# Performance work log

Hardware: AMD Instinct MI355X
Metric: run time of the kernel (lower is better)

## Reference

```python
import jax, jax.numpy as jnp
import numpy as np

B, L, HID, H, D = 1, 2048, 3072, 24, 128
MLP = 4 * HID
LH, LW = 32, 56      # latent mask grid -> LH*LW image tokens at the END of the sequence
LIP = 16             # IP-adapter image tokens
IP_SCALE = 0.6


def setup_inputs() -> dict:
    key = jax.random.key(0)
    k = jax.random.split(key, 10)
    # Flux rotary pe layout [1,1,L,D//2,2,2]: pe[...,0]=[cos,-sin], pe[...,1]=[sin,cos]
    pos = jnp.arange(L, dtype=jnp.float32)
    freqs = 1.0 / (10000.0 ** (jnp.arange(0, D, 2, dtype=jnp.float32) / D))
    ang = pos[:, None] * freqs[None, :]            # [L, D//2]
    cos, sin = jnp.cos(ang), jnp.sin(ang)
    pe = jnp.stack([jnp.stack([cos, -sin], -1), jnp.stack([sin, cos], -1)], -2)[None, None]
    return {
        "x": jax.random.normal(k[0], (B, L, HID), jnp.float32),
        "vec": jax.random.normal(k[1], (B, HID), jnp.float32),
        "pe": pe,
        "img_mask": jax.random.uniform(k[2], (B, LH, LW), jnp.float32),
        "image_emb": jax.random.normal(k[3], (B, LIP, HID), jnp.float32),
        "mod_w": jax.random.normal(k[4], (3 * HID, HID), jnp.float32) * 0.02,
        "mod_b": jnp.zeros((3 * HID,), jnp.float32),
        "lin1_w": jax.random.normal(k[5], (3 * HID + MLP, HID), jnp.float32) * 0.02,
        "lin1_b": jnp.zeros((3 * HID + MLP,), jnp.float32),
        "q_scale": jnp.ones((D,), jnp.float32),
        "k_scale": jnp.ones((D,), jnp.float32),
        "lin2_w": jax.random.normal(k[6], (HID, HID + MLP), jnp.float32) * 0.02,
        "lin2_b": jnp.zeros((HID,), jnp.float32),
        "ipk_w": jax.random.normal(k[7], (HID, HID), jnp.float32) * 0.02,
        "ipv_w": jax.random.normal(k[8], (HID, HID), jnp.float32) * 0.02,
    }


def _rms(x, scale, eps):
    # RMSNorm over last dim (QKNorm / norm_added_k)
    return x * jax.lax.rsqrt(jnp.mean(x * x, -1, keepdims=True) + eps) * scale


def _apply_rope(x, pe):
    # x: [B,H,L,D]; pe: [1,1,L,D//2,2,2]
    xr = x.reshape(x.shape[:-1] + (D // 2, 1, 2))
    out = pe[..., 0] * xr[..., 0] + pe[..., 1] * xr[..., 1]  # [B,H,L,D//2,2]
    return out.reshape(x.shape)


def _sdpa(q, k, v):
    # q:[B,H,Lq,D] k,v:[B,H,Lk,D] -> [B,Lq,H*D]
    s = jnp.einsum('bhqd,bhkd->bhqk', q, k) / jnp.sqrt(jnp.float32(D))
    o = jnp.einsum('bhqk,bhkd->bhqd', jax.nn.softmax(s, -1), v)
    return o.transpose(0, 2, 1, 3).reshape(q.shape[0], q.shape[2], H * D)


def reference(x, vec, pe, img_mask, image_emb, mod_w, mod_b, lin1_w, lin1_b,
              q_scale, k_scale, lin2_w, lin2_b, ipk_w, ipv_w):
    # modulation: SiLU(vec) -> Linear -> (shift, scale, gate), each [B,1,HID]
    mod = jax.nn.silu(vec) @ mod_w.T + mod_b
    shift, scale, gate = [m[:, None, :] for m in jnp.split(mod, 3, -1)]
    # pre_norm: LayerNorm, no affine, eps 1e-6 (biased variance, matches torch)
    ln = (x - jnp.mean(x, -1, keepdims=True)) * jax.lax.rsqrt(jnp.var(x, -1, keepdims=True) + 1e-6)
    x_mod = (1.0 + scale) * ln + shift
    # fused qkv + mlp projection
    h = x_mod @ lin1_w.T + lin1_b
    qkv, mlp = h[..., :3 * HID], h[..., 3 * HID:]
    q, k, v = qkv.reshape(B, L, 3, H, D).transpose(2, 0, 3, 1, 4)  # each [B,H,L,D]
    q = _rms(q, q_scale, 1e-6)
    k = _rms(k, k_scale, 1e-6)
    # rp_attention: RoPE then SDPA
    attn = _sdpa(_apply_rope(q, pe), _apply_rope(k, pe), v)       # [B,L,HID]
    # IP-adapter cross-attention: pre-rope q attends to projected image_emb
    ip_k = _rms((image_emb @ ipk_w.T).reshape(B, LIP, H, D).transpose(0, 2, 1, 3), 1.0, 1e-5)
    ip_v = (image_emb @ ipv_w.T).reshape(B, LIP, H, D).transpose(0, 2, 1, 3)
    ip_h = IP_SCALE * _sdpa(q, ip_k, ip_v)                        # [B,L,HID]
    # spatial mask applied to last LH*LW tokens, zeros elsewhere
    full_mask = jnp.concatenate(
        [jnp.zeros((B, L - LH * LW), ip_h.dtype), img_mask.reshape(B, LH * LW)], 1)
    attn = attn + ip_h * full_mask[..., None]
    out = jnp.concatenate([attn, jax.nn.gelu(mlp, approximate=True)], -1) @ lin2_w.T + lin2_b
    return x + gate * out
```

## Files before the change

### kernel.cpp

```cpp
#include <hip/hip_runtime.h>

#define HID 3072
#define LSEQ 2048
#define NH 24
#define HD 128
#define N1 21504
#define K2 15360

typedef unsigned short ushort_t;
typedef __attribute__((ext_vector_type(8))) short bf16x8;
typedef __attribute__((ext_vector_type(4))) float f32x4;

__device__ __forceinline__ unsigned short f2bf(float f) {
    union { float f; unsigned int u; } v; v.f = f;
    unsigned int u = v.u;
    u += 0x7fffu + ((u >> 16) & 1u);
    return (unsigned short)(u >> 16);
}
__device__ __forceinline__ float bf2f(unsigned short s) {
    union { unsigned int u; float f; } v; v.u = ((unsigned int)s) << 16;
    return v.f;
}
__device__ __forceinline__ float gelu_tanh(float x) {
    float u = 0.7978845608028654f * (x + 0.044715f * x * x * x);
    float t = 2.0f / (1.0f + __expf(-2.0f * u)) - 1.0f;
    return 0.5f * x * (1.0f + t);
}
__device__ __forceinline__ void gload_lds16(const ushort_t* g, ushort_t* l) {
    __builtin_amdgcn_global_load_lds((const __attribute__((address_space(1))) void*)g,
                                     (__attribute__((address_space(3))) void*)l, 16, 0, 0);
}

__global__ __launch_bounds__(256) void k_cvt(const float* __restrict__ src,
    ushort_t* __restrict__ dst, int n)
{
    int stride = gridDim.x * 256 * 8;
    for (int i = (blockIdx.x * 256 + threadIdx.x) * 8; i < n; i += stride) {
        float4 a = *reinterpret_cast<const float4*>(src + i);
        float4 b = *reinterpret_cast<const float4*>(src + i + 4);
        uint4 pk;
        pk.x = (unsigned)f2bf(a.x) | ((unsigned)f2bf(a.y) << 16);
        pk.y = (unsigned)f2bf(a.z) | ((unsigned)f2bf(a.w) << 16);
        pk.z = (unsigned)f2bf(b.x) | ((unsigned)f2bf(b.y) << 16);
        pk.w = (unsigned)f2bf(b.z) | ((unsigned)f2bf(b.w) << 16);
        *reinterpret_cast<uint4*>(dst + i) = pk;
    }
}

__global__ __launch_bounds__(256) void k_mod(const float* __restrict__ vec,
    const float* __restrict__ mw, const float* __restrict__ mb, float* __restrict__ mod) {
    __shared__ __align__(16) float sv[HID];
    int tid = threadIdx.x;
    for (int i = tid; i < HID; i += 256) {
        float v = vec[i];
        sv[i] = v / (1.0f + __expf(-v));
    }
    __syncthreads();
    int wave = tid >> 6, lane = tid & 63;
    int n = blockIdx.x * 4 + wave;
    const float* w = mw + (size_t)n * HID;
    float acc = 0.0f;
    for (int k = lane * 4; k < HID; k += 256) {
        float4 wv = *reinterpret_cast<const float4*>(w + k);
        float4 s  = *reinterpret_cast<const float4*>(sv + k);
        acc += wv.x * s.x + wv.y * s.y + wv.z * s.z + wv.w * s.w;
    }
    #pragma unroll
    for (int off = 1; off < 64; off <<= 1) acc += __shfl_xor(acc, off);
    if (lane == 0) mod[n] = acc + mb[n];
}

__global__ __launch_bounds__(256) void k_lnmod(const float* __restrict__ x,
    const float* __restrict__ mod, ushort_t* __restrict__ xmod) {
    int row = blockIdx.x, tid = threadIdx.x;
    const float4* xr = reinterpret_cast<const float4*>(x + (size_t)row * HID);
    float4 v[3];
    float s = 0.f, sq = 0.f;
    #pragma unroll
    for (int i = 0; i < 3; ++i) {
        v[i] = xr[tid + i * 256];
        s  += v[i].x + v[i].y + v[i].z + v[i].w;
        sq += v[i].x * v[i].x + v[i].y * v[i].y + v[i].z * v[i].z + v[i].w * v[i].w;
    }
    #pragma unroll
    for (int off = 1; off < 64; off <<= 1) { s += __shfl_xor(s, off); sq += __shfl_xor(sq, off); }
    __shared__ float rs[4], rq[4];
    int wave = tid >> 6, lane = tid & 63;
    if (lane == 0) { rs[wave] = s; rq[wave] = sq; }
    __syncthreads();
    s  = rs[0] + rs[1] + rs[2] + rs[3];
    sq = rq[0] + rq[1] + rq[2] + rq[3];
    float mean = s * (1.0f / HID);
    float var = sq * (1.0f / HID) - mean * mean;
    float rstd = rsqrtf(var + 1e-6f);
    ushort_t* orow = xmod + (size_t)row * HID;
    #pragma unroll
    for (int i = 0; i < 3; ++i) {
        int c = (tid + i * 256) * 4;
        float4 sc = *reinterpret_cast<const float4*>(mod + HID + c);
        float4 sh = *reinterpret_cast<const float4*>(mod + c);
        float o0 = (1.f + sc.x) * ((v[i].x - mean) * rstd) + sh.x;
        float o1 = (1.f + sc.y) * ((v[i].y - mean) * rstd) + sh.y;
        float o2 = (1.f + sc.z) * ((v[i].z - mean) * rstd) + sh.z;
        float o3 = (1.f + sc.w) * ((v[i].w - mean) * rstd) + sh.w;
        *reinterpret_cast<ushort4*>(orow + c) = make_ushort4(f2bf(o0), f2bf(o1), f2bf(o2), f2bf(o3));
    }
}

template<int EPI>
__global__ __launch_bounds__(512) void k_gemm8(
    const ushort_t* __restrict__ A, const ushort_t* __restrict__ W,
    const float* __restrict__ bias, int Ks, int klen,
    ushort_t* __restrict__ out_qkv, ushort_t* __restrict__ out_concat,
    float* __restrict__ part)
{
    extern __shared__ __align__(16) char smem_raw[];
    ushort_t* smem = (ushort_t*)smem_raw;
    int tid = threadIdx.x;
    int wid = tid >> 6, l = tid & 63;
    int wm = wid >> 2, wn = wid & 3;
    int lr = l & 15, lg = l >> 4;

    int NTILE = (EPI == 1) ? 84 : 12;
    int flat = blockIdx.y * NTILE + blockIdx.x;
    int nf = (flat & 7) * NTILE + (flat >> 3);
    int mt = nf & 7, nt = nf >> 3;
    int m0 = mt * 256, n0 = nt * 256;
    int koff = blockIdx.z * klen;
    int NT = klen >> 6;

    int lrow = l >> 3;
    int lc   = (l & 7) ^ lrow;
    int arow_st = wm * 128 + wn * 32 + lrow;
    int bhalf = wn >> 1, ridx = wm * 2 + (wn & 1);
    int brow_st = bhalf * 128 + ridx * 32 + lrow;
    const ushort_t* aSrc = A + (size_t)(m0 + arow_st) * Ks + koff + lc * 8;
    const ushort_t* bSrc = W + (size_t)(n0 + brow_st) * Ks + koff + lc * 8;
    int aDst = (wm * 128 + wn * 32) * 64;
    int bDst = (bhalf * 128 + ridx * 32) * 64;

    auto stageA = [&](int t, int buf, int c) {
        gload_lds16(aSrc + (size_t)c * 8 * Ks + (size_t)t * 64,
                    smem + buf * 16384 + aDst + c * 512);
    };
    auto stageB = [&](int t, int c) {
        gload_lds16(bSrc + (size_t)c * 8 * Ks + (size_t)t * 64,
                    smem + 49152 + (t & 1) * 16384 + bDst + c * 512);
    };
    auto readA = [&](int buf, int row, int ccc) {
        return *reinterpret_cast<const bf16x8*>(smem + buf * 16384 + row * 64 + ((ccc ^ (row & 7)) << 3));
    };
    auto readB = [&](int p, int row, int ccc) {
        return *reinterpret_cast<const bf16x8*>(smem + 49152 + p * 16384 + row * 64 + ((ccc ^ (row & 7)) << 3));
    };

    f32x4 acc[8][4] = {};
    bf16x8 bfrag[4][2];

    #pragma unroll
    for (int c = 0; c < 4; ++c) stageA(0, 0, c);
    #pragma unroll
    for (int c = 0; c < 4; ++c) stageB(0, c);
    #pragma unroll
    for (int c = 0; c < 4; ++c) stageA(1, 1, c);
    #pragma unroll
    for (int c = 0; c < 4; ++c) stageB(1, c);
    asm volatile("s_waitcnt vmcnt(8)" ::: "memory");
    __builtin_amdgcn_s_barrier();

    int pA = 0;
    int pA2 = 2;
    for (int t = 0; t < NT; ++t) {
        int pB = t & 1;
        #pragma unroll
        for (int ph = 0; ph < 4; ++ph) {
            bf16x8 af[2][2];
            if (ph == 0) {
                #pragma unroll
                for (int nj = 0; nj < 4; ++nj)
                    #pragma unroll
                    for (int kh = 0; kh < 2; ++kh)
                        bfrag[nj][kh] = readB(pB, wn * 64 + nj * 16 + lr, kh * 4 + lg);
            }
            #pragma unroll
            for (int i = 0; i < 2; ++i)
                #pragma unroll
                for (int kh = 0; kh < 2; ++kh)
                    af[i][kh] = readA(pA, wm * 128 + (2 * ph + i) * 16 + lr, kh * 4 + lg);
            if (ph < 2) {
                if (t + 2 < NT) { stageA(t + 2, pA2, ph * 2); stageA(t + 2, pA2, ph * 2 + 1); }
            } else {
                if (t + 2 < NT) { stageB(t + 2, (ph - 2) * 2); stageB(t + 2, (ph - 2) * 2 + 1); }
            }
            __builtin_amdgcn_s_barrier();
            __builtin_amdgcn_s_setprio(1);
            #pragma unroll
            for (int i = 0; i < 2; ++i)
                #pragma unroll
                for (int nj = 0; nj < 4; ++nj)
                    #pragma unroll
                    for (int kh = 0; kh < 2; ++kh)
                        acc[2 * ph + i][nj] = __builtin_amdgcn_mfma_f32_16x16x32_bf16(
                            af[i][kh], bfrag[nj][kh], acc[2 * ph + i][nj], 0, 0, 0);
            __builtin_amdgcn_s_setprio(0);
            if (ph == 3 && t + 1 < NT) {
                if (t + 2 < NT) asm volatile("s_waitcnt vmcnt(8)" ::: "memory");
                else            asm volatile("s_waitcnt vmcnt(0)" ::: "memory");
            }
            __builtin_amdgcn_s_barrier();
        }
        pA  = (pA  + 1 == 3) ? 0 : pA  + 1;
        pA2 = (pA2 + 1 == 3) ? 0 : pA2 + 1;
    }

    #pragma unroll
    for (int nj = 0; nj < 4; ++nj) {
        int col = n0 + wn * 64 + nj * 16 + lr;
        float b = (EPI == 1) ? bias[col] : 0.f;
        #pragma unroll
        for (int mi = 0; mi < 8; ++mi) {
            int rbase = m0 + wm * 128 + mi * 16 + lg * 4;
            #pragma unroll
            for (int r = 0; r < 4; ++r) {
                int mrow = rbase + r;
                float val = acc[mi][nj][r] + b;
                if (EPI == 1) {
                    if (col < 3 * HID) {
                        out_qkv[(size_t)mrow * (3 * HID) + col] = f2bf(val);
                    } else {
                        out_concat[(size_t)mrow * K2 + HID + (col - 3 * HID)] = f2bf(gelu_tanh(val));
                    }
                } else {
                    part[(size_t)blockIdx.z * LSEQ * HID + (size_t)mrow * HID + col] = val;
                }
            }
        }
    }
}

__global__ __launch_bounds__(256) void k_red(const float* __restrict__ part,
    const float* __restrict__ bias, const float* __restrict__ xres,
    const float* __restrict__ mod, float* __restrict__ dout)
{
    size_t base = ((size_t)blockIdx.x * 256 + threadIdx.x) * 4;
    int col = (int)(base % HID);
    float4 p0 = *reinterpret_cast<const float4*>(part + base);
    float4 p1 = *reinterpret_cast<const float4*>(part + (size_t)LSEQ * HID + base);
    float4 bb = *reinterpret_cast<const float4*>(bias + col);
    float4 gg = *reinterpret_cast<const float4*>(mod + 2 * HID + col);
    float4 xx = *reinterpret_cast<const float4*>(xres + base);
    float4 o;
    o.x = xx.x + gg.x * (p0.x + p1.x + bb.x);
    o.y = xx.y + gg.y * (p0.y + p1.y + bb.y);
    o.z = xx.z + gg.z * (p0.z + p1.z + bb.z);
    o.w = xx.w + gg.w * (p0.w + p1.w + bb.w);
    *reinterpret_cast<float4*>(dout + base) = o;
}

__global__ __launch_bounds__(256) void k_qkv(const ushort_t* __restrict__ qkv,
    const float* __restrict__ pe, const float* __restrict__ q_scale, const float* __restrict__ k_scale,
    ushort_t* __restrict__ q_rope, ushort_t* __restrict__ k_rope,
    ushort_t* __restrict__ q_rms, ushort_t* __restrict__ v_t)
{
    __shared__ ushort_t vtile[64][132];
    int h = blockIdx.y, l0 = blockIdx.x * 64;
    int wave = threadIdx.x >> 6, lane = threadIdx.x & 63;
    int d0 = lane * 2;
    float qs0 = q_scale[d0], qs1 = q_scale[d0 + 1];
    float ks0 = k_scale[d0], ks1 = k_scale[d0 + 1];
    for (int it = 0; it < 16; ++it) {
        int ll = it * 4 + wave;
        int l = l0 + ll;
        const ushort_t* base = qkv + (size_t)l * (3 * HID) + h * HD + d0;
        unsigned qw = *reinterpret_cast<const unsigned*>(base);
        unsigned kw = *reinterpret_cast<const unsigned*>(base + HID);
        unsigned vw = *reinterpret_cast<const unsigned*>(base + 2 * HID);
        float qx = bf2f((ushort_t)(qw & 0xffffu)), qy = bf2f((ushort_t)(qw >> 16));
        float kx = bf2f((ushort_t)(kw & 0xffffu)), ky = bf2f((ushort_t)(kw >> 16));
        float sq = qx * qx + qy * qy;
        float sk = kx * kx + ky * ky;
        #pragma unroll
        for (int off = 1; off < 64; off <<= 1) { sq += __shfl_xor(sq, off); sk += __shfl_xor(sk, off); }
        float rqv = rsqrtf(sq * (1.0f / HD) + 1e-6f);
        float rkv = rsqrtf(sk * (1.0f / HD) + 1e-6f);
        float qnx = qx * rqv * qs0, qny = qy * rqv * qs1;
        float knx = kx * rkv * ks0, kny = ky * rkv * ks1;
        float4 p = *reinterpret_cast<const float4*>(pe + ((size_t)l * 64 + lane) * 4);
        size_t off_hl = ((size_t)h * LSEQ + l) * HD + d0;
        *reinterpret_cast<unsigned*>(q_rms + off_hl) = (unsigned)f2bf(qnx) | ((unsigned)f2bf(qny) << 16);
        float qrx = p.x * qnx + p.y * qny, qry = p.z * qnx + p.w * qny;
        float krx = p.x * knx + p.y * kny, kry = p.z * knx + p.w * kny;
        *reinterpret_cast<unsigned*>(q_rope + off_hl) = (unsigned)f2bf(qrx) | ((unsigned)f2bf(qry) << 16);
        *reinterpret_cast<unsigned*>(k_rope + off_hl) = (unsigned)f2bf(krx) | ((unsigned)f2bf(kry) << 16);
        vtile[ll][d0] = (ushort_t)(vw & 0xffffu);
        vtile[ll][d0 + 1] = (ushort_t)(vw >> 16);
    }
    __syncthreads();
    int d = threadIdx.x >> 1, half = threadIdx.x & 1;
    ushort_t* dst = v_t + ((size_t)h * HD + d) * LSEQ + l0 + half * 32;
    #pragma unroll
    for (int g = 0; g < 4; ++g) {
        unsigned w0, w1, w2, w3;
        int lb = half * 32 + g * 8;
        w0 = (unsigned)vtile[lb + 0][d] | ((unsigned)vtile[lb + 1][d] << 16);
        w1 = (unsigned)vtile[lb + 2][d] | ((unsigned)vtile[lb + 3][d] << 16);
        w2 = (unsigned)vtile[lb + 4][d] | ((unsigned)vtile[lb + 5][d] << 16);
        w3 = (unsigned)vtile[lb + 6][d] | ((unsigned)vtile[lb + 7][d] << 16);
        reinterpret_cast<uint4*>(dst)[g] = make_uint4(w0, w1, w2, w3);
    }
}

__global__ __launch_bounds__(256) void k_ipgemv(const float* __restrict__ emb,
    const float* __restrict__ wk, const float* __restrict__ wv,
    float* __restrict__ ipk, float* __restrict__ ipv)
{
    int task = blockIdx.x * 4 + (threadIdx.x >> 6);
    int lane = threadIdx.x & 63;
    int which = task / HID;
    int n = task % HID;
    const float* w = (which ? wv : wk) + (size_t)n * HID;
    float acc[16];
    #pragma unroll
    for (int t = 0; t < 16; ++t) acc[t] = 0.f;
    for (int k = lane; k < HID; k += 64) {
        float wval = w[k];
        #pragma unroll
        for (int t = 0; t < 16; ++t) acc[t] += emb[t * HID + k] * wval;
    }
    #pragma unroll
    for (int off = 1; off < 64; off <<= 1) {
        #pragma unroll
        for (int t = 0; t < 16; ++t) acc[t] += __shfl_xor(acc[t], off);
    }
    if (lane == 0) {
        int hh = n >> 7, d = n & 127;
        float* dstp = which ? ipv : ipk;
        #pragma unroll
        for (int t = 0; t < 16; ++t) dstp[((size_t)hh * 16 + t) * HD + d] = acc[t];
    }
}

__global__ __launch_bounds__(256) void k_ipkrms(float* __restrict__ ipk) {
    int row = blockIdx.x * 4 + (threadIdx.x >> 6);
    int lane = threadIdx.x & 63;
    float2 v = *reinterpret_cast<const float2*>(ipk + (size_t)row * HD + lane * 2);
    float sq = v.x * v.x + v.y * v.y;
    #pragma unroll
    for (int off = 1; off < 64; off <<= 1) sq += __shfl_xor(sq, off);
    float r = rsqrtf(sq * (1.0f / HD) + 1e-5f);
    float2 o; o.x = v.x * r; o.y = v.y * r;
    *reinterpret_cast<float2*>(ipk + (size_t)row * HD + lane * 2) = o;
}

__global__ __launch_bounds__(256) void k_attn(const ushort_t* __restrict__ q_rope,
    const ushort_t* __restrict__ k_rope, const ushort_t* __restrict__ v_t,
    float* __restrict__ attnbuf)
{
    __shared__ __align__(16) ushort_t Ks[32 * 128];
    __shared__ __align__(16) ushort_t Vs[128 * 32];
    __shared__ __align__(16) ushort_t Ps[4 * 32 * 40];
    const float SC = 0.08838834764831845f;
    int h = blockIdx.y, q0 = blockIdx.x * 128;
    int tid = threadIdx.x, wave = tid >> 6, lane = tid & 63;
    int lr = lane & 15, lg = lane >> 4;
    const ushort_t* Kb = k_rope + (size_t)h * LSEQ * HD;
    const ushort_t* Vb = v_t + (size_t)h * HD * LSEQ;
    bf16x8 qf[2][4];
    #pragma unroll
    for (int i = 0; i < 2; ++i) {
        #pragma unroll
        for (int ks = 0; ks < 4; ++ks) {
            int row = q0 + wave * 32 + i * 16 + lr;
            int d = ks * 32 + lg * 8;
            qf[i][ks] = *reinterpret_cast<const bf16x8*>(q_rope + ((size_t)h * LSEQ + row) * HD + d);
        }
    }
    f32x4 o[2][8] = {};
    float mrun[2][4], lrun[2][4];
    #pragma unroll
    for (int i = 0; i < 2; ++i)
        #pragma unroll
        for (int r = 0; r < 4; ++r) { mrun[i][r] = -1e30f; lrun[i][r] = 0.f; }

    for (int kt = 0; kt < LSEQ; kt += 32) {
        #pragma unroll
        for (int ii = 0; ii < 2; ++ii) {
            int c = tid + ii * 256;
            int krow = c >> 4, kc = c & 15;
            uint4 va = *reinterpret_cast<const uint4*>(Kb + (size_t)(kt + krow) * HD + kc * 8);
            *reinterpret_cast<uint4*>(reinterpret_cast<char*>(Ks) + krow * 256 + ((kc ^ (krow & 15)) << 4)) = va;
            int dr = c >> 2, vc = c & 3;
            uint4 vb = *reinterpret_cast<const uint4*>(Vb + (size_t)dr * LSEQ + kt + vc * 8);
            *reinterpret_cast<uint4*>(reinterpret_cast<char*>(Vs) + dr * 64 + ((vc ^ ((dr >> 1) & 3)) << 4)) = vb;
        }
        __syncthreads();
        f32x4 s[2][2] = {};
        #pragma unroll
        for (int ks = 0; ks < 4; ++ks) {
            bf16x8 kf[2];
            #pragma unroll
            for (int j = 0; j < 2; ++j) {
                int krow = j * 16 + lr;
                int cc = ks * 4 + lg;
                kf[j] = *reinterpret_cast<const bf16x8*>(reinterpret_cast<char*>(Ks) + krow * 256 + ((cc ^ (krow & 15)) << 4));
            }
            #pragma unroll
            for (int i = 0; i < 2; ++i)
                #pragma unroll
                for (int j = 0; j < 2; ++j)
                    s[i][j] = __builtin_amdgcn_mfma_f32_16x16x32_bf16(qf[i][ks], kf[j], s[i][j], 0, 0, 0);
        }
        float alpha[2][4];
        #pragma unroll
        for (int i = 0; i < 2; ++i) {
            #pragma unroll
            for (int r = 0; r < 4; ++r) {
                float v0 = s[i][0][r] * SC, v1 = s[i][1][r] * SC;
                float mx = fmaxf(v0, v1);
                #pragma unroll
                for (int off = 1; off < 16; off <<= 1) mx = fmaxf(mx, __shfl_xor(mx, off));
                float mnew = fmaxf(mrun[i][r], mx);
                float al = __expf(mrun[i][r] - mnew);
                float p0 = __expf(v0 - mnew), p1 = __expf(v1 - mnew);
                float rs2 = p0 + p1;
                #pragma unroll
                for (int off = 1; off < 16; off <<= 1) rs2 += __shfl_xor(rs2, off);
                lrun[i][r] = lrun[i][r] * al + rs2;
                mrun[i][r] = mnew;
                alpha[i][r] = al;
                s[i][0][r] = p0; s[i][1][r] = p1;
            }
        }
        #pragma unroll
        for (int i = 0; i < 2; ++i)
            #pragma unroll
            for (int j8 = 0; j8 < 8; ++j8)
                #pragma unroll
                for (int r = 0; r < 4; ++r) o[i][j8][r] *= alpha[i][r];
        #pragma unroll
        for (int i = 0; i < 2; ++i)
            #pragma unroll
            for (int j = 0; j < 2; ++j)
                #pragma unroll
                for (int r = 0; r < 4; ++r) {
                    int ql = i * 16 + lg * 4 + r;
                    int kp = j * 16 + lr;
                    Ps[wave * 1280 + ql * 40 + kp] = f2bf(s[i][j][r]);
                }
        __syncthreads();
        bf16x8 pa[2];
        #pragma unroll
        for (int i = 0; i < 2; ++i)
            pa[i] = *reinterpret_cast<const bf16x8*>(Ps + wave * 1280 + (i * 16 + lr) * 40 + lg * 8);
        #pragma unroll
        for (int j8 = 0; j8 < 8; ++j8) {
            int d = j8 * 16 + lr;
            bf16x8 vf = *reinterpret_cast<const bf16x8*>(reinterpret_cast<char*>(Vs) + d * 64 + ((lg ^ ((d >> 1) & 3)) << 4));
            #pragma unroll
            for (int i = 0; i < 2; ++i)
                o[i][j8] = __builtin_amdgcn_mfma_f32_16x16x32_bf16(pa[i], vf, o[i][j8], 0, 0, 0);
        }
        __syncthreads();
    }
    #pragma unroll
    for (int i = 0; i < 2; ++i) {
        #pragma unroll
        for (int r = 0; r < 4; ++r) {
            float inv = 1.0f / lrun[i][r];
            int mrow = q0 + wave * 32 + i * 16 + lg * 4 + r;
            float* orow = attnbuf + (size_t)mrow * HID + h * HD;
            #pragma unroll
            for (int j8 = 0; j8 < 8; ++j8)
                orow[j8 * 16 + lr] = o[i][j8][r] * inv;
        }
    }
}

__global__ __launch_bounds__(256) void k_ipattn(const ushort_t* __restrict__ q_rms,
    const float* __restrict__ ipk, const float* __restrict__ ipv,
    const float* __restrict__ attnbuf, const float* __restrict__ img_mask,
    ushort_t* __restrict__ concat)
{
    int task = blockIdx.x * 4 + (threadIdx.x >> 6);
    int lane = threadIdx.x & 63;
    int h = task >> 11;
    int l = task & 2047;
    int d0 = lane * 2;
    float2 a = *reinterpret_cast<const float2*>(attnbuf + (size_t)l * HID + h * HD + d0);
    if (l >= 256) {
        float mask = img_mask[l - 256];
        unsigned qv = *reinterpret_cast<const unsigned*>(q_rms + ((size_t)h * LSEQ + l) * HD + d0);
        float qx = bf2f((unsigned short)(qv & 0xffffu)), qy = bf2f((unsigned short)(qv >> 16));
        float s[16];
        const float* kb = ipk + (size_t)h * 16 * HD + d0;
        #pragma unroll
        for (int j = 0; j < 16; ++j) {
            float2 kk = *reinterpret_cast<const float2*>(kb + j * HD);
            float part = qx * kk.x + qy * kk.y;
            #pragma unroll
            for (int off = 1; off < 64; off <<= 1) part += __shfl_xor(part, off);
            s[j] = part * 0.08838834764831845f;
        }
        float mx = s[0];
        #pragma unroll
        for (int j = 1; j < 16; ++j) mx = fmaxf(mx, s[j]);
        float sum = 0.f;
        #pragma unroll
        for (int j = 0; j < 16; ++j) { s[j] = __expf(s[j] - mx); sum += s[j]; }
        float ox = 0.f, oy = 0.f;
        const float* vb = ipv + (size_t)h * 16 * HD + d0;
        #pragma unroll
        for (int j = 0; j < 16; ++j) {
            float2 vv = *reinterpret_cast<const float2*>(vb + j * HD);
            ox += s[j] * vv.x; oy += s[j] * vv.y;
        }
        float f = 0.6f * mask / sum;
        a.x += f * ox; a.y += f * oy;
    }
    *reinterpret_cast<unsigned*>(concat + (size_t)l * K2 + h * HD + d0) =
        (unsigned)f2bf(a.x) | ((unsigned)f2bf(a.y) << 16);
}

extern "C" void kernel_launch(void* const* d_in, const int* in_sizes, int n_in,
                              void* d_out, int out_size, void* d_ws, size_t ws_size,
                              hipStream_t stream)
{
    (void)in_sizes; (void)n_in; (void)out_size; (void)ws_size;
    const float* x         = (const float*)d_in[0];
    const float* vec       = (const float*)d_in[1];
    const float* pe        = (const float*)d_in[2];
    const float* img_mask  = (const float*)d_in[3];
    const float* image_emb = (const float*)d_in[4];
    const float* mod_w     = (const float*)d_in[5];
    const float* mod_b     = (const float*)d_in[6];
    const float* lin1_w    = (const float*)d_in[7];
    const float* lin1_b    = (const float*)d_in[8];
    const float* q_scale   = (const float*)d_in[9];
    const float* k_scale   = (const float*)d_in[10];
    const float* lin2_w    = (const float*)d_in[11];
    const float* lin2_b    = (const float*)d_in[12];
    const float* ipk_w     = (const float*)d_in[13];
    const float* ipv_w     = (const float*)d_in[14];
    float* dout = (float*)d_out;

    char* wp = (char*)d_ws;
    auto alloc = [&](size_t bytes) { char* p = wp; wp += (bytes + 255) & ~(size_t)255; return p; };
    float*    mod     = (float*)   alloc((size_t)9216 * 4);
    ushort_t* xmod    = (ushort_t*)alloc((size_t)LSEQ * HID * 2);
    ushort_t* qkv     = (ushort_t*)alloc((size_t)LSEQ * 3 * HID * 2);
    ushort_t* concat  = (ushort_t*)alloc((size_t)LSEQ * K2 * 2);
    float*    attnbuf = (float*)   alloc((size_t)LSEQ * HID * 4);
    ushort_t* q_rope  = (ushort_t*)alloc((size_t)NH * LSEQ * HD * 2);
    ushort_t* k_rope  = (ushort_t*)alloc((size_t)NH * LSEQ * HD * 2);
    ushort_t* q_rms   = (ushort_t*)alloc((size_t)NH * LSEQ * HD * 2);
    ushort_t* v_t     = (ushort_t*)alloc((size_t)NH * HD * LSEQ * 2);
    float*    ipk     = (float*)   alloc((size_t)NH * 16 * HD * 4);
    float*    ipv     = (float*)   alloc((size_t)NH * 16 * HD * 4);
    ushort_t* lin1_bf = (ushort_t*)alloc((size_t)N1 * HID * 2);
    ushort_t* lin2_bf = (ushort_t*)alloc((size_t)HID * K2 * 2);
    float*    partial = (float*)   alloc((size_t)2 * LSEQ * HID * 4);

    hipFuncSetAttribute((const void*)k_gemm8<1>, hipFuncAttributeMaxDynamicSharedMemorySize, 163840);
    hipFuncSetAttribute((const void*)k_gemm8<0>, hipFuncAttributeMaxDynamicSharedMemorySize, 163840);

    k_cvt   <<<dim3(2048), dim3(256), 0, stream>>>(lin1_w, lin1_bf, N1 * HID);
    k_cvt   <<<dim3(2048), dim3(256), 0, stream>>>(lin2_w, lin2_bf, HID * K2);
    k_mod   <<<dim3(9216 / 4), dim3(256), 0, stream>>>(vec, mod_w, mod_b, mod);
    k_lnmod <<<dim3(LSEQ), dim3(256), 0, stream>>>(x, mod, xmod);
    k_gemm8<1><<<dim3(84, 8, 1), dim3(512), 163840, stream>>>(xmod, lin1_bf, lin1_b, HID, HID,
                                                              qkv, concat, nullptr);
    k_qkv   <<<dim3(32, NH), dim3(256), 0, stream>>>(qkv, pe, q_scale, k_scale,
                                                     q_rope, k_rope, q_rms, v_t);
    k_ipgemv<<<dim3(2 * HID / 4), dim3(256), 0, stream>>>(image_emb, ipk_w, ipv_w, ipk, ipv);
    k_ipkrms<<<dim3(NH * 16 / 4), dim3(256), 0, stream>>>(ipk);
    k_attn  <<<dim3(16, NH), dim3(256), 0, stream>>>(q_rope, k_rope, v_t, attnbuf);
    k_ipattn<<<dim3(NH * LSEQ / 4), dim3(256), 0, stream>>>(q_rms, ipk, ipv, attnbuf, img_mask, concat);
    k_gemm8<0><<<dim3(12, 8, 2), dim3(512), 163840, stream>>>(concat, lin2_bf, nullptr, K2, 7680,
                                                              nullptr, nullptr, partial);
    k_red   <<<dim3(LSEQ * HID / 1024), dim3(256), 0, stream>>>(partial, lin2_b, x, mod, dout);
}
```

Baseline: 1.134 ms.

## Restructure GEMM main loop with fewer barriers and raise lin2 split-K to 8

The GEMM inner loop drops its four barrier-separated phases per k-tile. It now loads all B fragments up front, interleaves A fragment reads and global-to-LDS staging with MFMA clusters, and uses only two barriers per tile. Separately, the second GEMM goes from 2-way to 8-way split-K, filling 768 blocks instead of 192, and the reduction kernel now sums 8 partials. The 8 fp32 partial buffers take more memory traffic, so the workspace is rearranged to alias the partials onto dead buffers.

```diff
diff --git a/kernel.cpp b/kernel.cpp
--- a/kernel.cpp
+++ b/kernel.cpp
@@ -106,6 +106,17 @@
         *reinterpret_cast<ushort4*>(orow + c) = make_ushort4(f2bf(o0), f2bf(o1), f2bf(o2), f2bf(o3));
     }
 }
+
+#define MFMA_CLUSTER(PH, AF)                                                          \
+    do {                                                                              \
+        __builtin_amdgcn_s_setprio(1);                                                \
+        _Pragma("unroll") for (int i_ = 0; i_ < 2; ++i_)                              \
+        _Pragma("unroll") for (int nj_ = 0; nj_ < 4; ++nj_)                           \
+        _Pragma("unroll") for (int kh_ = 0; kh_ < 2; ++kh_)                           \
+            acc[2 * (PH) + i_][nj_] = __builtin_amdgcn_mfma_f32_16x16x32_bf16(        \
+                AF[i_][kh_], bfrag[nj_][kh_], acc[2 * (PH) + i_][nj_], 0, 0, 0);      \
+        __builtin_amdgcn_s_setprio(0);                                                \
+    } while (0)
 
 template<int EPI>
 __global__ __launch_bounds__(512) void k_gemm8(
@@ -155,7 +166,6 @@
     };
 
     f32x4 acc[8][4] = {};
-    bf16x8 bfrag[4][2];
 
     #pragma unroll
     for (int c = 0; c < 4; ++c) stageA(0, 0, c);
@@ -172,43 +182,48 @@
     int pA2 = 2;
     for (int t = 0; t < NT; ++t) {
         int pB = t & 1;
-        #pragma unroll
-        for (int ph = 0; ph < 4; ++ph) {
-            bf16x8 af[2][2];
-            if (ph == 0) {
-                #pragma unroll
-                for (int nj = 0; nj < 4; ++nj)
-                    #pragma unroll
-                    for (int kh = 0; kh < 2; ++kh)
-                        bfrag[nj][kh] = readB(pB, wn * 64 + nj * 16 + lr, kh * 4 + lg);
-            }
-            #pragma unroll
-            for (int i = 0; i < 2; ++i)
-                #pragma unroll
-                for (int kh = 0; kh < 2; ++kh)
-                    af[i][kh] = readA(pA, wm * 128 + (2 * ph + i) * 16 + lr, kh * 4 + lg);
-            if (ph < 2) {
-                if (t + 2 < NT) { stageA(t + 2, pA2, ph * 2); stageA(t + 2, pA2, ph * 2 + 1); }
-            } else {
-                if (t + 2 < NT) { stageB(t + 2, (ph - 2) * 2); stageB(t + 2, (ph - 2) * 2 + 1); }
-            }
-            __builtin_amdgcn_s_barrier();
-            __builtin_amdgcn_s_setprio(1);
-            #pragma unroll
-            for (int i = 0; i < 2; ++i)
-                #pragma unroll
-                for (int nj = 0; nj < 4; ++nj)
-                    #pragma unroll
-                    for (int kh = 0; kh < 2; ++kh)
-                        acc[2 * ph + i][nj] = __builtin_amdgcn_mfma_f32_16x16x32_bf16(
-                            af[i][kh], bfrag[nj][kh], acc[2 * ph + i][nj], 0, 0, 0);
-            __builtin_amdgcn_s_setprio(0);
-            if (ph == 3 && t + 1 < NT) {
-                if (t + 2 < NT) asm volatile("s_waitcnt vmcnt(8)" ::: "memory");
-                else            asm volatile("s_waitcnt vmcnt(0)" ::: "memory");
-            }
-            __builtin_amdgcn_s_barrier();
-        }
+        bf16x8 bfrag[4][2], af0[2][2], af1[2][2], af2[2][2], af3[2][2];
+        #pragma unroll
+        for (int nj = 0; nj < 4; ++nj)
+            #pragma unroll
+            for (int kh = 0; kh < 2; ++kh)
+                bfrag[nj][kh] = readB(pB, wn * 64 + nj * 16 + lr, kh * 4 + lg);
+        #pragma unroll
+        for (int i = 0; i < 2; ++i)
+            #pragma unroll
+            for (int kh = 0; kh < 2; ++kh)
+                af0[i][kh] = readA(pA, wm * 128 + i * 16 + lr, kh * 4 + lg);
+        if (t + 2 < NT) {
+            stageA(t + 2, pA2, 0); stageA(t + 2, pA2, 1);
+            stageA(t + 2, pA2, 2); stageA(t + 2, pA2, 3);
+        }
+        #pragma unroll
+        for (int i = 0; i < 2; ++i)
+            #pragma unroll
+            for (int kh = 0; kh < 2; ++kh)
+                af1[i][kh] = readA(pA, wm * 128 + (2 + i) * 16 + lr, kh * 4 + lg);
+        MFMA_CLUSTER(0, af0);
+        #pragma unroll
+        for (int i = 0; i < 2; ++i)
+            #pragma unroll
+            for (int kh = 0; kh < 2; ++kh)
+                af2[i][kh] = readA(pA, wm * 128 + (4 + i) * 16 + lr, kh * 4 + lg);
+        MFMA_CLUSTER(1, af1);
+        __builtin_amdgcn_s_barrier();
+        if (t + 2 < NT) {
+            stageB(t + 2, 0); stageB(t + 2, 1);
+            stageB(t + 2, 2); stageB(t + 2, 3);
+        }
+        #pragma unroll
+        for (int i = 0; i < 2; ++i)
+            #pragma unroll
+            for (int kh = 0; kh < 2; ++kh)
+                af3[i][kh] = readA(pA, wm * 128 + (6 + i) * 16 + lr, kh * 4 + lg);
+        MFMA_CLUSTER(2, af2);
+        MFMA_CLUSTER(3, af3);
+        if (t + 2 < NT)      asm volatile("s_waitcnt vmcnt(8)" ::: "memory");
+        else if (t + 1 < NT) asm volatile("s_waitcnt vmcnt(0)" ::: "memory");
+        __builtin_amdgcn_s_barrier();
         pA  = (pA  + 1 == 3) ? 0 : pA  + 1;
         pA2 = (pA2 + 1 == 3) ? 0 : pA2 + 1;
     }
@@ -244,16 +259,20 @@
 {
     size_t base = ((size_t)blockIdx.x * 256 + threadIdx.x) * 4;
     int col = (int)(base % HID);
-    float4 p0 = *reinterpret_cast<const float4*>(part + base);
-    float4 p1 = *reinterpret_cast<const float4*>(part + (size_t)LSEQ * HID + base);
+    float4 s = *reinterpret_cast<const float4*>(part + base);
+    #pragma unroll
+    for (int z = 1; z < 8; ++z) {
+        float4 p = *reinterpret_cast<const float4*>(part + (size_t)z * LSEQ * HID + base);
+        s.x += p.x; s.y += p.y; s.z += p.z; s.w += p.w;
+    }
     float4 bb = *reinterpret_cast<const float4*>(bias + col);
     float4 gg = *reinterpret_cast<const float4*>(mod + 2 * HID + col);
     float4 xx = *reinterpret_cast<const float4*>(xres + base);
     float4 o;
-    o.x = xx.x + gg.x * (p0.x + p1.x + bb.x);
-    o.y = xx.y + gg.y * (p0.y + p1.y + bb.y);
-    o.z = xx.z + gg.z * (p0.z + p1.z + bb.z);
-    o.w = xx.w + gg.w * (p0.w + p1.w + bb.w);
+    o.x = xx.x + gg.x * (s.x + bb.x);
+    o.y = xx.y + gg.y * (s.y + bb.y);
+    o.z = xx.z + gg.z * (s.z + bb.z);
+    o.w = xx.w + gg.w * (s.w + bb.w);
     *reinterpret_cast<float4*>(dout + base) = o;
 }
 
@@ -546,19 +565,20 @@
     char* wp = (char*)d_ws;
     auto alloc = [&](size_t bytes) { char* p = wp; wp += (bytes + 255) & ~(size_t)255; return p; };
     float*    mod     = (float*)   alloc((size_t)9216 * 4);
+    ushort_t* concat  = (ushort_t*)alloc((size_t)LSEQ * K2 * 2);
+    ushort_t* lin2_bf = (ushort_t*)alloc((size_t)HID * K2 * 2);
+    float*    ipk     = (float*)   alloc((size_t)NH * 16 * HD * 4);
+    float*    ipv     = (float*)   alloc((size_t)NH * 16 * HD * 4);
+    char* ubase = wp;
+    ushort_t* lin1_bf = (ushort_t*)alloc((size_t)N1 * HID * 2);
     ushort_t* xmod    = (ushort_t*)alloc((size_t)LSEQ * HID * 2);
     ushort_t* qkv     = (ushort_t*)alloc((size_t)LSEQ * 3 * HID * 2);
-    ushort_t* concat  = (ushort_t*)alloc((size_t)LSEQ * K2 * 2);
     float*    attnbuf = (float*)   alloc((size_t)LSEQ * HID * 4);
     ushort_t* q_rope  = (ushort_t*)alloc((size_t)NH * LSEQ * HD * 2);
     ushort_t* k_rope  = (ushort_t*)alloc((size_t)NH * LSEQ * HD * 2);
     ushort_t* q_rms   = (ushort_t*)alloc((size_t)NH * LSEQ * HD * 2);
     ushort_t* v_t     = (ushort_t*)alloc((size_t)NH * HD * LSEQ * 2);
-    float*    ipk     = (float*)   alloc((size_t)NH * 16 * HD * 4);
-    float*    ipv     = (float*)   alloc((size_t)NH * 16 * HD * 4);
-    ushort_t* lin1_bf = (ushort_t*)alloc((size_t)N1 * HID * 2);
-    ushort_t* lin2_bf = (ushort_t*)alloc((size_t)HID * K2 * 2);
-    float*    partial = (float*)   alloc((size_t)2 * LSEQ * HID * 4);
+    float*    partial = (float*)ubase;
 
     hipFuncSetAttribute((const void*)k_gemm8<1>, hipFuncAttributeMaxDynamicSharedMemorySize, 163840);
     hipFuncSetAttribute((const void*)k_gemm8<0>, hipFuncAttributeMaxDynamicSharedMemorySize, 163840);
@@ -575,7 +595,7 @@
     k_ipkrms<<<dim3(NH * 16 / 4), dim3(256), 0, stream>>>(ipk);
     k_attn  <<<dim3(16, NH), dim3(256), 0, stream>>>(q_rope, k_rope, v_t, attnbuf);
     k_ipattn<<<dim3(NH * LSEQ / 4), dim3(256), 0, stream>>>(q_rms, ipk, ipv, attnbuf, img_mask, concat);
-    k_gemm8<0><<<dim3(12, 8, 2), dim3(512), 163840, stream>>>(concat, lin2_bf, nullptr, K2, 7680,
+    k_gemm8<0><<<dim3(12, 8, 8), dim3(512), 163840, stream>>>(concat, lin2_bf, nullptr, K2, 1920,
                                                               nullptr, nullptr, partial);
     k_red   <<<dim3(LSEQ * HID / 1024), dim3(256), 0, stream>>>(partial, lin2_b, x, mod, dout);
 }
```

Result: slower. 1.160 ms (+2.3%).
